# Performance work log

Measured on AMD Instinct MI355X. Metric: run time of the kernel, lower is better.

The kernel has to match this reference:

```python
import jax, jax.numpy as jnp
import numpy as np

L, H, K, N_IN, B = 8, 512, 16, 512, 8192  # layers, nodes/layer, fan-in, input nodes, batch


def setup_inputs() -> dict:
    key = jax.random.key(0)
    k_x, k_w, k_b = jax.random.split(key, 3)
    x = jax.random.normal(k_x, (B, N_IN), dtype=jnp.float32)
    # DAG links: node in layer l may read any of the N_IN + l*H previously computed nodes
    rng = np.random.default_rng(0)
    link_idx = np.stack(
        [rng.integers(0, N_IN + l * H, size=(H, K)) for l in range(L)]
    ).astype(np.int32)  # [L, H, K]
    weights = jax.random.normal(k_w, (L, H, K), dtype=jnp.float32) * 0.3
    bias = jax.random.normal(k_b, (L, H), dtype=jnp.float32) * 0.1
    return {"x": x, "link_idx": jnp.asarray(link_idx), "weights": weights, "bias": bias}


def reference(x, link_idx, weights, bias):
    # values dict -> growing [B, n_nodes_so_far] buffer; per-node Linear(K,1)+Sigmoid
    values = x  # [B, N_IN]
    for l in range(L):  # small fixed structural loop over topological layers
        g = values[:, link_idx[l]]                      # gather predecessor values [B, H, K]
        out = jax.nn.sigmoid(
            jnp.einsum("bhk,hk->bh", g, weights[l]) + bias[l]
        )                                               # [B, H]
        values = jnp.concatenate([values, out], axis=1)
    return values[:, -H:]  # output nodes = last layer
```

## Files before the change

### kernel.cpp

```cpp
#include <hip/hip_runtime.h>
#include <hip/hip_fp16.h>

#define LAYERS 8
#define H      512
#define K      16
#define N_IN   512
#define BATCH  8192
#define R      8
#define NT     512
#define LDS_COLS 4096


__global__ __launch_bounds__(NT, 2)
void ffn_fused_kernel(const float* __restrict__ x,
                      const int*   __restrict__ link_idx,
                      const float* __restrict__ weights,
                      const float* __restrict__ bias,
                      float*       __restrict__ out)
{
    __shared__ __align__(16) __half vals[LDS_COLS * R];

    const int tid  = threadIdx.x;
    const int row0 = blockIdx.x * R;

    {
        const int c = tid;
        float v[R];
        #pragma unroll
        for (int r = 0; r < R; ++r)
            v[r] = x[(row0 + r) * N_IN + c];
        __half2 p[R / 2];
        #pragma unroll
        for (int r = 0; r < R / 2; ++r)
            p[r] = __floats2half2_rn(v[2 * r], v[2 * r + 1]);
        *(uint4*)&vals[c * R] = *(const uint4*)p;
    }

    int   idxA[K]; float wA[K]; float bA;
    {
        const int base = tid * K;
        #pragma unroll
        for (int q = 0; q < 4; ++q) {
            *(int4*)  &idxA[4 * q] = ((const int4*)  (link_idx + base))[q];
            *(float4*)&wA  [4 * q] = ((const float4*)(weights  + base))[q];
        }
        bA = bias[tid];
    }

    __syncthreads();

    #pragma unroll
    for (int l = 0; l < LAYERS; ++l) {
        int idxB[K]; float wB[K]; float bB = 0.0f;
        if (l < LAYERS - 1) {
            const int nb = ((l + 1) * H + tid) * K;
            #pragma unroll
            for (int q = 0; q < 4; ++q) {
                *(int4*)  &idxB[4 * q] = ((const int4*)  (link_idx + nb))[q];
                *(float4*)&wB  [4 * q] = ((const float4*)(weights  + nb))[q];
            }
            bB = bias[(l + 1) * H + tid];
        }

        float acc[R];
        #pragma unroll
        for (int r = 0; r < R; ++r) acc[r] = bA;

        #pragma unroll
        for (int k = 0; k < K; ++k) {
            const uint4 g = *(const uint4*)&vals[idxA[k] * R];
            const __half2* hp = (const __half2*)&g;
            const float wk = wA[k];
            #pragma unroll
            for (int r = 0; r < R / 2; ++r) {
                const float2 f = __half22float2(hp[r]);
                acc[2 * r]     = fmaf(f.x, wk, acc[2 * r]);
                acc[2 * r + 1] = fmaf(f.y, wk, acc[2 * r + 1]);
            }
        }

        #pragma unroll
        for (int r = 0; r < R; ++r)
            acc[r] = __builtin_amdgcn_rcpf(1.0f + __expf(-acc[r]));

        if (l < LAYERS - 1) {
            __half2 p[R / 2];
            #pragma unroll
            for (int r = 0; r < R / 2; ++r)
                p[r] = __floats2half2_rn(acc[2 * r], acc[2 * r + 1]);
            *(uint4*)&vals[(N_IN + l * H + tid) * R] = *(const uint4*)p;
            __syncthreads();
            #pragma unroll
            for (int k = 0; k < K; ++k) { idxA[k] = idxB[k]; wA[k] = wB[k]; }
            bA = bB;
        } else {
            #pragma unroll
            for (int r = 0; r < R; ++r)
                out[(row0 + r) * H + tid] = acc[r];
        }
    }
}

extern "C" void kernel_launch(void* const* d_in, const int* in_sizes, int n_in,
                              void* d_out, int out_size, void* d_ws, size_t ws_size,
                              hipStream_t stream) {
    const float* x        = (const float*)d_in[0];
    const int*   link_idx = (const int*)  d_in[1];
    const float* weights  = (const float*)d_in[2];
    const float* bias     = (const float*)d_in[3];
    float*       out      = (float*)d_out;

    ffn_fused_kernel<<<dim3(BATCH / R), dim3(NT), 0, stream>>>(x, link_idx, weights, bias, out);
}
```

Baseline: 109.9 us.

## Presort and rotate link indices per node to reduce LDS bank conflicts

Adds a small prep kernel that reorders each node's K links by LDS bank group (index mod 8), rotates the order by thread id, and stores byte offsets that are already scaled. The main kernel then reads these prepared indices and weights, so its address arithmetic gets simpler and the 16-byte LDS gathers made at the same time by neighbouring threads are meant to spread across banks. The cost is one extra kernel launch plus writing and re-reading the permuted parameters through the workspace each call. The original path remains as a fallback when no workspace is given.

```diff
diff --git a/kernel.cpp b/kernel.cpp
--- a/kernel.cpp
+++ b/kernel.cpp
@@ -9,12 +9,52 @@
 #define R      8
 #define NT     512
 #define LDS_COLS 4096
+#define PARAM_N  (LAYERS * H * K)
 
 
+__global__ __launch_bounds__(512)
+void ffn_prep_kernel(const int*   __restrict__ link_idx,
+                     const float* __restrict__ weights,
+                     int*         __restrict__ idx2,
+                     float*       __restrict__ w2)
+{
+    const int t    = blockIdx.x * 512 + threadIdx.x;
+    const int base = t * K;
+
+    int idx[K]; float w[K];
+    #pragma unroll
+    for (int k = 0; k < K; ++k) { idx[k] = link_idx[base + k]; w[k] = weights[base + k]; }
+
+    int cnt[8];
+    #pragma unroll
+    for (int p = 0; p < 8; ++p) cnt[p] = 0;
+    #pragma unroll
+    for (int k = 0; k < K; ++k) cnt[idx[k] & 7]++;
+    int ofs[8]; int s = 0;
+    #pragma unroll
+    for (int p = 0; p < 8; ++p) { ofs[p] = s; s += cnt[p]; }
+    int sid[K]; float sw[K];
+    #pragma unroll
+    for (int k = 0; k < K; ++k) {
+        const int p = idx[k] & 7;
+        const int d = ofs[p]++;
+        sid[d] = idx[k]; sw[d] = w[k];
+    }
+
+    const int rot = t & 15;
+    #pragma unroll
+    for (int j = 0; j < K; ++j) {
+        const int srcslot = (j + rot) & 15;
+        idx2[base + j] = sid[srcslot] << 4;
+        w2[base + j]  = sw[srcslot];
+    }
+}
+
+template <int PRESCALED>
 __global__ __launch_bounds__(NT, 2)
 void ffn_fused_kernel(const float* __restrict__ x,
-                      const int*   __restrict__ link_idx,
-                      const float* __restrict__ weights,
+                      const int*   __restrict__ idxp,
+                      const float* __restrict__ wp,
                       const float* __restrict__ bias,
                       float*       __restrict__ out)
 {
@@ -41,8 +81,12 @@
         const int base = tid * K;
         #pragma unroll
         for (int q = 0; q < 4; ++q) {
-            *(int4*)  &idxA[4 * q] = ((const int4*)  (link_idx + base))[q];
-            *(float4*)&wA  [4 * q] = ((const float4*)(weights  + base))[q];
+            *(int4*)  &idxA[4 * q] = ((const int4*)  (idxp + base))[q];
+            *(float4*)&wA  [4 * q] = ((const float4*)(wp   + base))[q];
+        }
+        if (!PRESCALED) {
+            #pragma unroll
+            for (int k = 0; k < K; ++k) idxA[k] <<= 4;
         }
         bA = bias[tid];
     }
@@ -56,8 +100,12 @@
             const int nb = ((l + 1) * H + tid) * K;
             #pragma unroll
             for (int q = 0; q < 4; ++q) {
-                *(int4*)  &idxB[4 * q] = ((const int4*)  (link_idx + nb))[q];
-                *(float4*)&wB  [4 * q] = ((const float4*)(weights  + nb))[q];
+                *(int4*)  &idxB[4 * q] = ((const int4*)  (idxp + nb))[q];
+                *(float4*)&wB  [4 * q] = ((const float4*)(wp   + nb))[q];
+            }
+            if (!PRESCALED) {
+                #pragma unroll
+                for (int k = 0; k < K; ++k) idxB[k] <<= 4;
             }
             bB = bias[(l + 1) * H + tid];
         }
@@ -68,7 +116,7 @@
 
         #pragma unroll
         for (int k = 0; k < K; ++k) {
-            const uint4 g = *(const uint4*)&vals[idxA[k] * R];
+            const uint4 g = *(const uint4*)((const char*)vals + idxA[k]);
             const __half2* hp = (const __half2*)&g;
             const float wk = wA[k];
             #pragma unroll
@@ -110,5 +158,14 @@
     const float* bias     = (const float*)d_in[3];
     float*       out      = (float*)d_out;
 
-    ffn_fused_kernel<<<dim3(BATCH / R), dim3(NT), 0, stream>>>(x, link_idx, weights, bias, out);
+    const size_t need = 2 * (size_t)PARAM_N * 4;
+
+    if (d_ws != nullptr && ws_size >= need) {
+        int*   idx2 = (int*)d_ws;
+        float* w2   = (float*)((char*)d_ws + PARAM_N * sizeof(int));
+        ffn_prep_kernel<<<dim3(LAYERS), dim3(512), 0, stream>>>(link_idx, weights, idx2, w2);
+        ffn_fused_kernel<1><<<dim3(BATCH / R), dim3(NT), 0, stream>>>(x, idx2, w2, bias, out);
+    } else {
+        ffn_fused_kernel<0><<<dim3(BATCH / R), dim3(NT), 0, stream>>>(x, link_idx, weights, bias, out);
+    }
 }
```

Result: slower. 118.6 us (+7.9%).
